# Kernel tuning notes

Measured on AMD Instinct MI355X. Metric: run time of the kernel, lower is better.

The kernel has to match this reference:

```python
import jax, jax.numpy as jnp
import numpy as np

B, T, E, H = 4, 4096, 1024, 16
D = E // H          # per-head hidden_size in fla LinearAttention (num_heads=1)
CH = 64             # fused-chunk chunk size


def setup_inputs() -> dict:
    key = jax.random.key(0)
    k1, k2, k3, k4, k5 = jax.random.split(key, 5)
    s = 1.0 / np.sqrt(D).astype(np.float32)
    x = jax.random.normal(k1, (B, T, E), dtype=jnp.float32)
    Wq = jax.random.normal(k2, (D, D), dtype=jnp.float32) * s
    Wk = jax.random.normal(k3, (D, D), dtype=jnp.float32) * s
    Wv = jax.random.normal(k4, (D, D), dtype=jnp.float32) * s
    Wo = jax.random.normal(k5, (D, D), dtype=jnp.float32) * s
    return {"x": x, "Wq": Wq, "Wk": Wk, "Wv": Wv, "Wo": Wo}


def _phi(x):
    # fla 'elu' feature map: elu(x) + 1 (positive features)
    return jax.nn.elu(x) + 1.0


def _linear_attn_fused_chunk(q, k, v):
    # q,k,v: [B,H,T,D]; causal linear attention via chunked recurrence.
    b, h, t, d = q.shape
    n = t // CH
    # [N, B, H, CH, D] so scan runs over chunks
    qc = q.reshape(b, h, n, CH, d).transpose(2, 0, 1, 3, 4)
    kc = k.reshape(b, h, n, CH, d).transpose(2, 0, 1, 3, 4)
    vc = v.reshape(b, h, n, CH, d).transpose(2, 0, 1, 3, 4)
    mask = jnp.tril(jnp.ones((CH, CH), dtype=q.dtype))  # causal, diag inclusive

    def step(S, inp):
        qi, ki, vi = inp                                   # [B,H,CH,D]
        attn = jnp.einsum('bhck,bhek->bhce', qi, ki) * mask  # intra-chunk scores
        o_intra = jnp.einsum('bhce,bhed->bhcd', attn, vi)
        o_inter = jnp.einsum('bhck,bhkd->bhcd', qi, S)       # past-state term
        S_new = S + jnp.einsum('bhck,bhcd->bhkd', ki, vi)    # state update
        return S_new, o_intra + o_inter

    S0 = jnp.zeros((b, h, d, d), dtype=q.dtype)
    _, oc = jax.lax.scan(step, S0, (qc, kc, vc))           # oc: [N,B,H,CH,D]
    return oc.transpose(1, 2, 0, 3, 4).reshape(b, h, t, d)


def reference(x, Wq, Wk, Wv, Wo):
    # split outer heads: [B,T,E] -> [B,H,T,D]
    xh = x.reshape(B, T, H, D).transpose(0, 2, 1, 3)
    # shared [D,D] projections (fla LinearAttention with num_heads=1), tied elu feature map on q,k
    q = _phi(jnp.einsum('bhtd,de->bhte', xh, Wq))
    k = _phi(jnp.einsum('bhtd,de->bhte', xh, Wk))
    v = jnp.einsum('bhtd,de->bhte', xh, Wv)
    o = _linear_attn_fused_chunk(q, k, v)                  # no feature-map norm, identity output norm
    o = jnp.einsum('bhtd,de->bhte', o, Wo)
    return o.transpose(0, 2, 1, 3).reshape(B, T, E)
```

## Files before the change

kernel.cpp:

```cpp
#include <hip/hip_runtime.h>
#include <cstdint>
#include <cstddef>

constexpr int Bc = 4, Tc = 4096, Ec = 1024, Hc = 16, Dc = 64, CHc = 64;
constexpr int NSEG = 16;
constexpr int SEGT = Tc / NSEG;
constexpr int NCHUNK = SEGT / CHc;

typedef __attribute__((ext_vector_type(8))) short short8;
typedef __attribute__((ext_vector_type(4))) float f32x4;

__device__ __forceinline__ unsigned short* sws(unsigned short* b, int row, int colbyte) {
  return (unsigned short*)((char*)b + (row << 7) + (colbyte ^ ((row & 7) << 4)));
}

__device__ __forceinline__ unsigned short f2bf(float f) {
  union { float f; unsigned int u; } v; v.f = f;
  return (unsigned short)((v.u + 0x7FFFu + ((v.u >> 16) & 1u)) >> 16);
}
__device__ __forceinline__ unsigned int pk2(float lo, float hi) {
  union { float f; unsigned int u; } a, b; a.f = lo; b.f = hi;
  return __builtin_amdgcn_perm(b.u + 0x8000u, a.u + 0x8000u, 0x07060302u);
}
__device__ __forceinline__ float bf2f(unsigned int u16) {
  union { unsigned int u; float f; } v; v.u = u16 << 16;
  return v.f;
}
__device__ __forceinline__ float phi_elu1(float x) {
  return x > 0.f ? x + 1.f : __expf(x);
}
__device__ __forceinline__ short8 ld8(const unsigned short* p) {
  return *reinterpret_cast<const short8*>(p);
}
__device__ __forceinline__ short8 pk8(float4 a, float4 b) {
  union { unsigned int u[4]; short8 s; } r;
  r.u[0] = pk2(a.x, a.y); r.u[1] = pk2(a.z, a.w);
  r.u[2] = pk2(b.x, b.y); r.u[3] = pk2(b.z, b.w);
  return r.s;
}
__device__ __forceinline__ void st4(unsigned short* p, float v0, float v1, float v2, float v3) {
  uint2 t; t.x = pk2(v0, v1); t.y = pk2(v2, v3);
  *reinterpret_cast<uint2*>(p) = t;
}

#define MFMA(a, b, c) __builtin_amdgcn_mfma_f32_16x16x32_bf16((a), (b), (c), 0, 0, 0)

__global__ __launch_bounds__(256) void prep_weights(
    const float* __restrict__ Wq, const float* __restrict__ Wk,
    const float* __restrict__ Wv, const float* __restrict__ Wo,
    unsigned short* __restrict__ wbuf) {
  __shared__ float s_wvT[4096];
  __shared__ float s_wo[4096];
  const int tid = threadIdx.x;
  const int i = blockIdx.x * 256 + tid;
  for (int j = tid; j < 4096; j += 256) {
    s_wvT[(j & 63) * 64 + (j >> 6)] = Wv[j];
    s_wo[j] = Wo[j];
  }
  __syncthreads();
  const int r = i >> 6, c = i & 63;
  wbuf[c * 64 + r] = f2bf(Wq[i]);
  wbuf[4096 + c * 64 + r] = f2bf(Wk[i]);
  float acc = 0.f;
  for (int g = 0; g < 64; ++g)
    acc += s_wvT[g * 64 + c] * s_wo[g * 64 + r];
  wbuf[8192 + i] = f2bf(acc);
}

__global__ __launch_bounds__(256, 3) void pass1_kvseg(
    const float* __restrict__ x, const unsigned short* __restrict__ wbuf,
    unsigned short* __restrict__ kvseg) {
  __shared__ unsigned short s_kT[2][4096];
  __shared__ unsigned short s_vT[2][4096];
  const int tid = threadIdx.x, w = tid >> 6, lane = tid & 63, lr = lane & 15, lq = lane >> 4;
  const int bh = blockIdx.x, sg = blockIdx.y, b = bh >> 4, h = bh & 15;
  const float* xbase = x + ((size_t)b * Tc + (size_t)sg * SEGT) * Ec + h * Dc;
  const unsigned short* wkT = wbuf + 4096;
  const unsigned short* wvoT = wbuf + 8192;
  const f32x4 Z = {0.f, 0.f, 0.f, 0.f};

  short8 bwk[4][2], bwv[4][2];
#pragma unroll
  for (int c = 0; c < 4; ++c)
#pragma unroll
    for (int kk = 0; kk < 2; ++kk) {
      bwk[c][kk] = ld8(wkT + (c * 16 + lr) * 64 + kk * 32 + lq * 8);
      bwv[c][kk] = ld8(wvoT + (c * 16 + lr) * 64 + kk * 32 + lq * 8);
    }

  const float* xr = xbase + (size_t)(w * 16 + lr) * Ec + lq * 8;
  float4 p0 = ((const float4*)xr)[0], p1 = ((const float4*)xr)[1];
  float4 p2 = ((const float4*)(xr + 32))[0], p3 = ((const float4*)(xr + 32))[1];

  f32x4 sacc[4] = {Z, Z, Z, Z};
#pragma unroll
  for (int ci = 0; ci < NCHUNK; ++ci) {
    unsigned short* skT = s_kT[ci & 1];
    unsigned short* svT = s_vT[ci & 1];
    short8 xa0 = pk8(p0, p1), xa1 = pk8(p2, p3);
    if (ci < NCHUNK - 1) {
      const float* nr = xbase + (size_t)((ci + 1) * CHc + w * 16 + lr) * Ec + lq * 8;
      p0 = ((const float4*)nr)[0]; p1 = ((const float4*)nr)[1];
      p2 = ((const float4*)(nr + 32))[0]; p3 = ((const float4*)(nr + 32))[1];
    }
    f32x4 ak[4] = {Z, Z, Z, Z}, av[4] = {Z, Z, Z, Z};
    __builtin_amdgcn_s_setprio(1);
#pragma unroll
    for (int c = 0; c < 4; ++c) {
      ak[c] = MFMA(xa0, bwk[c][0], ak[c]); ak[c] = MFMA(xa1, bwk[c][1], ak[c]);
      av[c] = MFMA(xa0, bwv[c][0], av[c]); av[c] = MFMA(xa1, bwv[c][1], av[c]);
    }
    __builtin_amdgcn_s_setprio(0);
#pragma unroll
    for (int c = 0; c < 4; ++c) {
      st4(sws(skT, c * 16 + lr, w * 32 + lq * 8),
          phi_elu1(ak[c][0]), phi_elu1(ak[c][1]), phi_elu1(ak[c][2]), phi_elu1(ak[c][3]));
      st4(sws(svT, c * 16 + lr, w * 32 + lq * 8), av[c][0], av[c][1], av[c][2], av[c][3]);
    }
    __syncthreads();

    short8 akt0 = ld8(sws(skT, w * 16 + lr, lq * 16));
    short8 akt1 = ld8(sws(skT, w * 16 + lr, 64 + lq * 16));
    __builtin_amdgcn_s_setprio(1);
#pragma unroll
    for (int c = 0; c < 4; ++c) {
      sacc[c] = MFMA(akt0, ld8(sws(svT, c * 16 + lr, lq * 16)), sacc[c]);
      sacc[c] = MFMA(akt1, ld8(sws(svT, c * 16 + lr, 64 + lq * 16)), sacc[c]);
    }
    __builtin_amdgcn_s_setprio(0);
  }

  unsigned short* dst = kvseg + ((size_t)bh * NSEG + sg) * 4096 + (w * 64 + lane) * 16;
#pragma unroll
  for (int c = 0; c < 4; ++c) {
    uint2 t; t.x = pk2(sacc[c][0], sacc[c][1]); t.y = pk2(sacc[c][2], sacc[c][3]);
    *reinterpret_cast<uint2*>(dst + c * 4) = t;
  }
}

__global__ __launch_bounds__(256, 2) void pass3_main(
    const float* __restrict__ x, const unsigned short* __restrict__ wbuf,
    const unsigned short* __restrict__ kvseg, float* __restrict__ out) {
  __shared__ unsigned short s_x [4096];
  __shared__ unsigned short s_q [4096];
  __shared__ unsigned short s_k [4096];
  __shared__ unsigned short s_kT[4096];
  __shared__ unsigned short s_vT[4096];
  __shared__ unsigned short s_Sb[4096];

  const int tid = threadIdx.x, w = tid >> 6, lane = tid & 63, lr = lane & 15, lq = lane >> 4;
  const int bh = blockIdx.x, sg = blockIdx.y, b = bh >> 4, h = bh & 15;
  const float* xbase = x + ((size_t)b * Tc + (size_t)sg * SEGT) * Ec + h * Dc;
  float* obase = out + ((size_t)b * Tc + (size_t)sg * SEGT) * Ec + h * Dc;
  const unsigned short* wqT = wbuf;
  const unsigned short* wkT = wbuf + 4096;
  const unsigned short* wvoT = wbuf + 8192;
  const int sr = tid >> 2, sc = tid & 3;
  const f32x4 Z = {0.f, 0.f, 0.f, 0.f};

  f32x4 sacc[4] = {Z, Z, Z, Z};
  {
    const unsigned short* kvb = kvseg + (size_t)bh * NSEG * 4096 + (w * 64 + lane) * 16;
    for (int sp = 0; sp < sg; ++sp) {
      const unsigned short* p = kvb + (size_t)sp * 4096;
#pragma unroll
      for (int c = 0; c < 4; ++c) {
        uint2 u = *reinterpret_cast<const uint2*>(p + c * 4);
        sacc[c][0] += bf2f(u.x & 0xFFFFu); sacc[c][1] += bf2f(u.x >> 16);
        sacc[c][2] += bf2f(u.y & 0xFFFFu); sacc[c][3] += bf2f(u.y >> 16);
      }
    }
  }

  short8 awq[2], awk[2], bwk[4][2], bwv[4][2];
#pragma unroll
  for (int kk = 0; kk < 2; ++kk) {
    awq[kk] = ld8(wqT + (w * 16 + lr) * 64 + kk * 32 + lq * 8);
    awk[kk] = ld8(wkT + (w * 16 + lr) * 64 + kk * 32 + lq * 8);
  }
#pragma unroll
  for (int c = 0; c < 4; ++c)
#pragma unroll
    for (int kk = 0; kk < 2; ++kk) {
      bwk[c][kk] = ld8(wkT + (c * 16 + lr) * 64 + kk * 32 + lq * 8);
      bwv[c][kk] = ld8(wvoT + (c * 16 + lr) * 64 + kk * 32 + lq * 8);
    }

  {
    const float4* xf = (const float4*)(xbase + (size_t)sr * Ec + sc * 16);
    float4 f0 = xf[0], f1 = xf[1], f2 = xf[2], f3 = xf[3];
    *(short8*)sws(s_x, sr, sc * 32) = pk8(f0, f1);
    *(short8*)sws(s_x, sr, sc * 32 + 16) = pk8(f2, f3);
  }
  __syncthreads();

#pragma unroll
  for (int ci = 0; ci < NCHUNK; ++ci) {
    float4 pf0, pf1, pf2, pf3;
    if (ci < NCHUNK - 1) {
      const float4* xf = (const float4*)(xbase + (size_t)((ci + 1) * CHc + sr) * Ec + sc * 16);
      pf0 = xf[0]; pf1 = xf[1]; pf2 = xf[2]; pf3 = xf[3];
    }

    short8 xb[4][2];
#pragma unroll
    for (int c = 0; c < 4; ++c) {
      xb[c][0] = ld8(sws(s_x, c * 16 + lr, lq * 16));
      xb[c][1] = ld8(sws(s_x, c * 16 + lr, 64 + lq * 16));
    }
    short8 xw0 = ld8(sws(s_x, w * 16 + lr, lq * 16));
    short8 xw1 = ld8(sws(s_x, w * 16 + lr, 64 + lq * 16));
#pragma unroll
    for (int c = 0; c < 4; ++c)
      st4(sws(s_Sb, c * 16 + lr, w * 32 + lq * 8), sacc[c][0], sacc[c][1], sacc[c][2], sacc[c][3]);

    f32x4 aqt[4] = {Z, Z, Z, Z}, akt[4] = {Z, Z, Z, Z}, ack[4] = {Z, Z, Z, Z}, acv[4] = {Z, Z, Z, Z};
    __builtin_amdgcn_s_setprio(1);
#pragma unroll
    for (int c = 0; c < 4; ++c) {
      aqt[c] = MFMA(awq[0], xb[c][0], aqt[c]); aqt[c] = MFMA(awq[1], xb[c][1], aqt[c]);
      akt[c] = MFMA(awk[0], xb[c][0], akt[c]); akt[c] = MFMA(awk[1], xb[c][1], akt[c]);
      ack[c] = MFMA(xw0, bwk[c][0], ack[c]);   ack[c] = MFMA(xw1, bwk[c][1], ack[c]);
      acv[c] = MFMA(xw0, bwv[c][0], acv[c]);   acv[c] = MFMA(xw1, bwv[c][1], acv[c]);
    }
    __builtin_amdgcn_s_setprio(0);
#pragma unroll
    for (int c = 0; c < 4; ++c) {
      const int row = c * 16 + lr, cb = w * 32 + lq * 8;
      st4(sws(s_q, row, cb), phi_elu1(aqt[c][0]), phi_elu1(aqt[c][1]), phi_elu1(aqt[c][2]), phi_elu1(aqt[c][3]));
      st4(sws(s_k, row, cb), phi_elu1(akt[c][0]), phi_elu1(akt[c][1]), phi_elu1(akt[c][2]), phi_elu1(akt[c][3]));
      st4(sws(s_kT, row, cb), phi_elu1(ack[c][0]), phi_elu1(ack[c][1]), phi_elu1(ack[c][2]), phi_elu1(ack[c][3]));
      st4(sws(s_vT, row, cb), acv[c][0], acv[c][1], acv[c][2], acv[c][3]);
    }
    __syncthreads();

    short8 a_q0 = ld8(sws(s_q, w * 16 + lr, lq * 16));
    short8 a_q1 = ld8(sws(s_q, w * 16 + lr, 64 + lq * 16));
    short8 a_k0 = ld8(sws(s_k, w * 16 + lr, lq * 16));
    short8 a_k1 = ld8(sws(s_k, w * 16 + lr, 64 + lq * 16));
    short8 a_t0 = ld8(sws(s_kT, w * 16 + lr, lq * 16));
    short8 a_t1 = ld8(sws(s_kT, w * 16 + lr, 64 + lq * 16));
    f32x4 aat[4] = {Z, Z, Z, Z}, ao[4] = {Z, Z, Z, Z};
    __builtin_amdgcn_s_setprio(1);
#pragma unroll
    for (int c = 0; c < 4; ++c) {
      const int row = c * 16 + lr;
      aat[c]  = MFMA(a_k0, ld8(sws(s_q, row, lq * 16)), aat[c]);
      aat[c]  = MFMA(a_k1, ld8(sws(s_q, row, 64 + lq * 16)), aat[c]);
      ao[c]   = MFMA(a_q0, ld8(sws(s_Sb, row, lq * 16)), ao[c]);
      ao[c]   = MFMA(a_q1, ld8(sws(s_Sb, row, 64 + lq * 16)), ao[c]);
      sacc[c] = MFMA(a_t0, ld8(sws(s_vT, row, lq * 16)), sacc[c]);
      sacc[c] = MFMA(a_t1, ld8(sws(s_vT, row, 64 + lq * 16)), sacc[c]);
    }
    __builtin_amdgcn_s_setprio(0);
#pragma unroll
    for (int c = 0; c < 4; ++c) {
      int t = c * 16 + lr, tp = w * 16 + lq * 4;
      float m0 = (tp + 0 <= t) ? aat[c][0] : 0.f;
      float m1 = (tp + 1 <= t) ? aat[c][1] : 0.f;
      float m2 = (tp + 2 <= t) ? aat[c][2] : 0.f;
      float m3 = (tp + 3 <= t) ? aat[c][3] : 0.f;
      st4(sws(s_x, t, tp * 2), m0, m1, m2, m3);
    }
    __syncthreads();

    short8 a_a0 = ld8(sws(s_x, w * 16 + lr, lq * 16));
    short8 a_a1 = ld8(sws(s_x, w * 16 + lr, 64 + lq * 16));
    __builtin_amdgcn_s_setprio(1);
#pragma unroll
    for (int c = 0; c < 4; ++c) {
      const int row = c * 16 + lr;
      ao[c] = MFMA(a_a0, ld8(sws(s_vT, row, lq * 16)), ao[c]);
      ao[c] = MFMA(a_a1, ld8(sws(s_vT, row, 64 + lq * 16)), ao[c]);
    }
    __builtin_amdgcn_s_setprio(0);
    float* orow = obase + (size_t)(ci * CHc) * Ec;
#pragma unroll
    for (int c = 0; c < 4; ++c)
#pragma unroll
      for (int j = 0; j < 4; ++j)
        orow[(size_t)(w * 16 + lq * 4 + j) * Ec + c * 16 + lr] = ao[c][j];
    if (ci < NCHUNK - 1) {
      *(short8*)sws(s_x, sr, sc * 32) = pk8(pf0, pf1);
      *(short8*)sws(s_x, sr, sc * 32 + 16) = pk8(pf2, pf3);
    }
    __syncthreads();
  }
}

extern "C" void kernel_launch(void* const* d_in, const int* in_sizes, int n_in,
                              void* d_out, int out_size, void* d_ws, size_t ws_size,
                              hipStream_t stream) {
  const float* x  = (const float*)d_in[0];
  const float* Wq = (const float*)d_in[1];
  const float* Wk = (const float*)d_in[2];
  const float* Wv = (const float*)d_in[3];
  const float* Wo = (const float*)d_in[4];
  float* out = (float*)d_out;

  unsigned short* wbuf  = (unsigned short*)d_ws;
  unsigned short* kvseg = (unsigned short*)((char*)d_ws + 32768);

  prep_weights<<<dim3(16), dim3(256), 0, stream>>>(Wq, Wk, Wv, Wo, wbuf);
  pass1_kvseg<<<dim3(64, NSEG), dim3(256), 0, stream>>>(x, wbuf, kvseg);
  pass3_main<<<dim3(64, NSEG), dim3(256), 0, stream>>>(x, wbuf, kvseg, out);
}
```

Baseline: 67.75 us.

## Cut pass3 LDS and registers for higher occupancy; skip unused last segment state

Pass3 now raises its launch bound to 4 blocks per CU. It drops two LDS buffers by staging k and kT through one per-wave scratch tile with scalar transposed stores, and stops keeping the Wv/o weight fragments in registers, reloading them from global memory each chunk instead. The projection MFMAs are split into sequential phases so fewer accumulators are live at once. Pass1 also no longer computes the last segment's state, which no later segment reads. The cost is more scalar LDS stores, repeated weight loads, and a possible race on the reused scratch tile within a wave.

```diff
diff --git a/kernel.cpp b/kernel.cpp
--- a/kernel.cpp
+++ b/kernel.cpp
@@ -21,6 +21,10 @@
 __device__ __forceinline__ unsigned int pk2(float lo, float hi) {
   union { float f; unsigned int u; } a, b; a.f = lo; b.f = hi;
   return __builtin_amdgcn_perm(b.u + 0x8000u, a.u + 0x8000u, 0x07060302u);
+}
+__device__ __forceinline__ unsigned short h1(float f) {
+  union { float f; unsigned int u; } v; v.f = f;
+  return (unsigned short)((v.u + 0x8000u) >> 16);
 }
 __device__ __forceinline__ float bf2f(unsigned int u16) {
   union { unsigned int u; float f; } v; v.u = u16 << 16;
@@ -118,7 +122,6 @@
       st4(sws(svT, c * 16 + lr, w * 32 + lq * 8), av[c][0], av[c][1], av[c][2], av[c][3]);
     }
     __syncthreads();
-
     short8 akt0 = ld8(sws(skT, w * 16 + lr, lq * 16));
     short8 akt1 = ld8(sws(skT, w * 16 + lr, 64 + lq * 16));
     __builtin_amdgcn_s_setprio(1);
@@ -138,15 +141,14 @@
   }
 }
 
-__global__ __launch_bounds__(256, 2) void pass3_main(
+__global__ __launch_bounds__(256, 4) void pass3_main(
     const float* __restrict__ x, const unsigned short* __restrict__ wbuf,
     const unsigned short* __restrict__ kvseg, float* __restrict__ out) {
   __shared__ unsigned short s_x [4096];
   __shared__ unsigned short s_q [4096];
-  __shared__ unsigned short s_k [4096];
-  __shared__ unsigned short s_kT[4096];
   __shared__ unsigned short s_vT[4096];
   __shared__ unsigned short s_Sb[4096];
+  __shared__ unsigned short s_scr[4096];
 
   const int tid = threadIdx.x, w = tid >> 6, lane = tid & 63, lr = lane & 15, lq = lane >> 4;
   const int bh = blockIdx.x, sg = blockIdx.y, b = bh >> 4, h = bh & 15;
@@ -172,7 +174,7 @@
     }
   }
 
-  short8 awq[2], awk[2], bwk[4][2], bwv[4][2];
+  short8 awq[2], awk[2], bwk[4][2];
 #pragma unroll
   for (int kk = 0; kk < 2; ++kk) {
     awq[kk] = ld8(wqT + (w * 16 + lr) * 64 + kk * 32 + lq * 8);
@@ -181,10 +183,8 @@
 #pragma unroll
   for (int c = 0; c < 4; ++c)
 #pragma unroll
-    for (int kk = 0; kk < 2; ++kk) {
+    for (int kk = 0; kk < 2; ++kk)
       bwk[c][kk] = ld8(wkT + (c * 16 + lr) * 64 + kk * 32 + lq * 8);
-      bwv[c][kk] = ld8(wvoT + (c * 16 + lr) * 64 + kk * 32 + lq * 8);
-    }
 
   {
     const float4* xf = (const float4*)(xbase + (size_t)sr * Ec + sc * 16);
@@ -196,50 +196,62 @@
 
 #pragma unroll
   for (int ci = 0; ci < NCHUNK; ++ci) {
+    short8 xw0 = ld8(sws(s_x, w * 16 + lr, lq * 16));
+    short8 xw1 = ld8(sws(s_x, w * 16 + lr, 64 + lq * 16));
+#pragma unroll
+    for (int c = 0; c < 4; ++c)
+      st4(sws(s_Sb, c * 16 + lr, w * 32 + lq * 8), sacc[c][0], sacc[c][1], sacc[c][2], sacc[c][3]);
+
+    __builtin_amdgcn_s_setprio(1);
+#pragma unroll
+    for (int c = 0; c < 4; ++c) {
+      short8 xb0 = ld8(sws(s_x, c * 16 + lr, lq * 16));
+      short8 xb1 = ld8(sws(s_x, c * 16 + lr, 64 + lq * 16));
+      f32x4 aqt = Z, akt = Z;
+      aqt = MFMA(awq[0], xb0, aqt); aqt = MFMA(awq[1], xb1, aqt);
+      akt = MFMA(awk[0], xb0, akt); akt = MFMA(awk[1], xb1, akt);
+      st4(sws(s_q, c * 16 + lr, w * 32 + lq * 8),
+          phi_elu1(aqt[0]), phi_elu1(aqt[1]), phi_elu1(aqt[2]), phi_elu1(aqt[3]));
+#pragma unroll
+      for (int j = 0; j < 4; ++j)
+        *sws(s_scr, w * 16 + lq * 4 + j, (c * 16 + lr) * 2) = h1(phi_elu1(akt[j]));
+    }
+    __builtin_amdgcn_s_setprio(0);
+    short8 a_t0 = ld8(sws(s_scr, w * 16 + lr, lq * 16));
+    short8 a_t1 = ld8(sws(s_scr, w * 16 + lr, 64 + lq * 16));
+
+    __builtin_amdgcn_s_setprio(1);
+#pragma unroll
+    for (int c = 0; c < 4; ++c) {
+      f32x4 ack = Z;
+      ack = MFMA(xw0, bwk[c][0], ack); ack = MFMA(xw1, bwk[c][1], ack);
+#pragma unroll
+      for (int j = 0; j < 4; ++j)
+        *sws(s_scr, w * 16 + lq * 4 + j, (c * 16 + lr) * 2) = h1(phi_elu1(ack[j]));
+    }
+    __builtin_amdgcn_s_setprio(0);
+    short8 a_k0 = ld8(sws(s_scr, w * 16 + lr, lq * 16));
+    short8 a_k1 = ld8(sws(s_scr, w * 16 + lr, 64 + lq * 16));
+
+    __builtin_amdgcn_s_setprio(1);
+#pragma unroll
+    for (int c = 0; c < 4; ++c) {
+      short8 bv0 = ld8(wvoT + (c * 16 + lr) * 64 + lq * 8);
+      short8 bv1 = ld8(wvoT + (c * 16 + lr) * 64 + 32 + lq * 8);
+      f32x4 acv = Z;
+      acv = MFMA(xw0, bv0, acv); acv = MFMA(xw1, bv1, acv);
+      st4(sws(s_vT, c * 16 + lr, w * 32 + lq * 8), acv[0], acv[1], acv[2], acv[3]);
+    }
+    __builtin_amdgcn_s_setprio(0);
+    __syncthreads();
+
     float4 pf0, pf1, pf2, pf3;
     if (ci < NCHUNK - 1) {
       const float4* xf = (const float4*)(xbase + (size_t)((ci + 1) * CHc + sr) * Ec + sc * 16);
       pf0 = xf[0]; pf1 = xf[1]; pf2 = xf[2]; pf3 = xf[3];
     }
-
-    short8 xb[4][2];
-#pragma unroll
-    for (int c = 0; c < 4; ++c) {
-      xb[c][0] = ld8(sws(s_x, c * 16 + lr, lq * 16));
-      xb[c][1] = ld8(sws(s_x, c * 16 + lr, 64 + lq * 16));
-    }
-    short8 xw0 = ld8(sws(s_x, w * 16 + lr, lq * 16));
-    short8 xw1 = ld8(sws(s_x, w * 16 + lr, 64 + lq * 16));
-#pragma unroll
-    for (int c = 0; c < 4; ++c)
-      st4(sws(s_Sb, c * 16 + lr, w * 32 + lq * 8), sacc[c][0], sacc[c][1], sacc[c][2], sacc[c][3]);
-
-    f32x4 aqt[4] = {Z, Z, Z, Z}, akt[4] = {Z, Z, Z, Z}, ack[4] = {Z, Z, Z, Z}, acv[4] = {Z, Z, Z, Z};
-    __builtin_amdgcn_s_setprio(1);
-#pragma unroll
-    for (int c = 0; c < 4; ++c) {
-      aqt[c] = MFMA(awq[0], xb[c][0], aqt[c]); aqt[c] = MFMA(awq[1], xb[c][1], aqt[c]);
-      akt[c] = MFMA(awk[0], xb[c][0], akt[c]); akt[c] = MFMA(awk[1], xb[c][1], akt[c]);
-      ack[c] = MFMA(xw0, bwk[c][0], ack[c]);   ack[c] = MFMA(xw1, bwk[c][1], ack[c]);
-      acv[c] = MFMA(xw0, bwv[c][0], acv[c]);   acv[c] = MFMA(xw1, bwv[c][1], acv[c]);
-    }
-    __builtin_amdgcn_s_setprio(0);
-#pragma unroll
-    for (int c = 0; c < 4; ++c) {
-      const int row = c * 16 + lr, cb = w * 32 + lq * 8;
-      st4(sws(s_q, row, cb), phi_elu1(aqt[c][0]), phi_elu1(aqt[c][1]), phi_elu1(aqt[c][2]), phi_elu1(aqt[c][3]));
-      st4(sws(s_k, row, cb), phi_elu1(akt[c][0]), phi_elu1(akt[c][1]), phi_elu1(akt[c][2]), phi_elu1(akt[c][3]));
-      st4(sws(s_kT, row, cb), phi_elu1(ack[c][0]), phi_elu1(ack[c][1]), phi_elu1(ack[c][2]), phi_elu1(ack[c][3]));
-      st4(sws(s_vT, row, cb), acv[c][0], acv[c][1], acv[c][2], acv[c][3]);
-    }
-    __syncthreads();
-
     short8 a_q0 = ld8(sws(s_q, w * 16 + lr, lq * 16));
     short8 a_q1 = ld8(sws(s_q, w * 16 + lr, 64 + lq * 16));
-    short8 a_k0 = ld8(sws(s_k, w * 16 + lr, lq * 16));
-    short8 a_k1 = ld8(sws(s_k, w * 16 + lr, 64 + lq * 16));
-    short8 a_t0 = ld8(sws(s_kT, w * 16 + lr, lq * 16));
-    short8 a_t1 = ld8(sws(s_kT, w * 16 + lr, 64 + lq * 16));
     f32x4 aat[4] = {Z, Z, Z, Z}, ao[4] = {Z, Z, Z, Z};
     __builtin_amdgcn_s_setprio(1);
 #pragma unroll
@@ -302,6 +314,6 @@
   unsigned short* kvseg = (unsigned short*)((char*)d_ws + 32768);
 
   prep_weights<<<dim3(16), dim3(256), 0, stream>>>(Wq, Wk, Wv, Wo, wbuf);
-  pass1_kvseg<<<dim3(64, NSEG), dim3(256), 0, stream>>>(x, wbuf, kvseg);
+  pass1_kvseg<<<dim3(64, NSEG - 1), dim3(256), 0, stream>>>(x, wbuf, kvseg);
   pass3_main<<<dim3(64, NSEG), dim3(256), 0, stream>>>(x, wbuf, kvseg, out);
 }
```

After: 149.9 us. 2.21x slower.
